# Kernel optimization log

Measured on AMD Instinct MI355X. Metric: run time of the kernel, lower is better.

## Reference

```python
import jax, jax.numpy as jnp
import numpy as np

B, S, D = 4, 2048, 1024
NEG = 1e9


def setup_inputs() -> dict:
    key = jax.random.key(0)
    ks = jax.random.split(key, 4)
    scale = 1.0 / np.sqrt(D)  # glorot-ish init scale for stability
    x = jax.random.normal(ks[0], (B, S, D), dtype=jnp.float32)
    Wq = jax.random.normal(ks[1], (D, D), dtype=jnp.float32) * scale
    Wk = jax.random.normal(ks[2], (D, D), dtype=jnp.float32) * scale
    Wv = jax.random.normal(ks[3], (D, D), dtype=jnp.float32) * scale
    bq = jnp.zeros((D,), jnp.float32)
    bk = jnp.zeros((D,), jnp.float32)
    bv = jnp.zeros((D,), jnp.float32)
    return {"x": x, "Wq": Wq, "bq": bq, "Wk": Wk, "bk": bk, "Wv": Wv, "bv": bv}


def reference(x, Wq, bq, Wk, bk, Wv, bv):
    # Dense projections (single head, no 1/sqrt(d) scaling, matching source)
    q = x @ Wq + bq                      # [B,S,D]
    k = x @ Wk + bk                      # [B,S,D]
    v = x @ Wv + bv                      # [B,S,D]
    scores = jnp.einsum('bqd,bkd->bqk', q, k)   # [B,S,S]
    seq = scores.shape[-1]
    mask = jnp.tril(jnp.ones((seq, seq), scores.dtype))  # lower-triangular causal
    scores = scores * mask - NEG * (1.0 - mask)
    weights = jax.nn.softmax(scores, axis=-1)
    return jnp.einsum('bqk,bkd->bqd', weights, v)
```

## Files before the change

kernel.cpp:

```cpp
#include <hip/hip_runtime.h>

typedef float f32x4  __attribute__((ext_vector_type(4)));
typedef _Float16 f16x8  __attribute__((ext_vector_type(8)));
typedef _Float16 f16x4v __attribute__((ext_vector_type(4)));
typedef _Float16 f16x8v __attribute__((ext_vector_type(8)));

__device__ inline void load_lds16(const _Float16* g, _Float16* l) {
    __builtin_amdgcn_global_load_lds((const __attribute__((address_space(1))) void*)g,
                                     (__attribute__((address_space(3))) void*)l, 16, 0, 0);
}

__global__ __launch_bounds__(256)
void convert_h(const float* __restrict__ X, _Float16* __restrict__ H, long n4)
{
    long i = (long)blockIdx.x * 256 + threadIdx.x;
    if (i >= n4) return;
    f32x4 v = ((const f32x4*)X)[i];
    f16x4v h;
#pragma unroll
    for (int k = 0; k < 4; ++k) h[k] = (_Float16)v[k];
    ((f16x4v*)H)[i] = h;
}

__global__ __launch_bounds__(256)
void transpose_w3(const float* __restrict__ Wq, const float* __restrict__ Wk,
                  const float* __restrict__ Wv,
                  _Float16* __restrict__ W2, _Float16* __restrict__ Wvt, int D)
{
    const int z = blockIdx.z;
    const float* W = (z == 0) ? Wq : (z == 1) ? Wk : Wv;

    __shared__ float t[32][33];
    const int tid = threadIdx.x;
    const int bx = blockIdx.x * 32, by = blockIdx.y * 32;
    const int c = tid & 31, r0 = tid >> 5;
#pragma unroll
    for (int r = r0; r < 32; r += 8)
        t[r][c] = W[(long)(by + r) * D + bx + c];
    __syncthreads();
#pragma unroll
    for (int r = r0; r < 32; r += 8) {
        float v = t[c][r];
        _Float16 h = (_Float16)v;
        if (z < 2) {
            const long nrow = (long)z * D + bx + r;
            W2[nrow * 2 * D + by + c]     = h;
            W2[nrow * 2 * D + D + by + c] = (_Float16)(v - (float)h);
        } else {
            Wvt[(long)(bx + r) * D + by + c] = h;
        }
    }
}

#define STAGES_T(NTHR, NQ, gb, ld, base0, kbase, dst)                           \
    {                                                                           \
        _Pragma("unroll")                                                       \
        for (int q_ = 0; q_ < (NQ); ++q_) {                                     \
            const int p_ = q_ * (NTHR) + tid;                                   \
            const int rp_ = p_ >> 3;                                            \
            const int gl_ = (p_ & 7) ^ (rp_ & 7);                               \
            const int row_ = rp_ + ((gl_ >> 2) << 7);                           \
            load_lds16((gb) + (long)((base0) + row_) * (ld) + (kbase) +         \
                           ((gl_ & 3) << 3),                                    \
                       (dst) + p_ * 8);                                         \
        }                                                                       \
    }

__global__ __launch_bounds__(512)
void proj8(const _Float16* __restrict__ x_h, const _Float16* __restrict__ W2,
           const _Float16* __restrict__ Wvt,
           _Float16* __restrict__ Q_h, _Float16* __restrict__ Khl,
           _Float16* __restrict__ Vt,
           const float* __restrict__ bq, const float* __restrict__ bk,
           const float* __restrict__ bv)
{
    constexpr int D = 1024, SEQ = 2048;
    __shared__ __align__(16) _Float16 lds[65536];

    const int orig = blockIdx.x;
    const bool isV = orig >= 256;
    int ct, rt, ldb, NT2;
    const _Float16* Bb;
    if (!isV) {
        const int x = orig & 7, i = orig >> 3;
        rt = x * 4 + (i & 3);  ct = i >> 2;
        Bb = W2;  ldb = 2 * D; NT2 = 64;
    } else {
        const int o = orig - 256, x = o & 7, i = o >> 3;
        rt = x * 4 + (i & 3);  ct = i >> 2;
        Bb = Wvt; ldb = D;     NT2 = 32;
    }
    const int row0 = rt * 256, col0 = ct * 256;

    const int tid = threadIdx.x;
    const int wave = tid >> 6, lane = tid & 63, l16 = lane & 15, quad = lane >> 4;
    const int wmh = (wave >> 2) * 128;
    const int wn  = (wave & 3) * 64;
    const int ahalf = (wave >> 2) << 2;

    STAGES_T(512, 2, x_h, D, row0, 0,  lds);
    STAGES_T(512, 2, Bb, ldb, col0, 0, lds + 32768);
    STAGES_T(512, 2, x_h, D, row0, 32, lds + 8192);
    STAGES_T(512, 2, Bb, ldb, col0, 32, lds + 32768 + 8192);
    asm volatile("s_waitcnt vmcnt(4)" ::: "memory");
    __builtin_amdgcn_s_barrier();

    f32x4 acc[8][4] = {};

    for (int s = 0; s < NT2; ++s) {
        _Float16* Asl = lds + (s & 3) * 8192;
        _Float16* Bsl = lds + 32768 + (s & 3) * 8192;
        const bool pf = (s + 2 < NT2);
        const int kA2 = ((s + 2) * 32) & (D - 1);
        const int kB2 = (s + 2) * 32;

        f16x8 b[4], a0[4];
#pragma unroll
        for (int j = 0; j < 4; ++j) {
            const int nr = wn + j * 16 + l16;
            const int rpb = nr & 127;
            const int gpb = ((((nr >> 7) << 2) | quad) ^ (rpb & 7));
            b[j] = *(const f16x8*)&Bsl[rpb * 64 + gpb * 8];
        }
#pragma unroll
        for (int il = 0; il < 4; ++il) {
            const int rp = il * 16 + l16;
            const int gpa = ((ahalf | quad) ^ (rp & 7));
            a0[il] = *(const f16x8*)&Asl[rp * 64 + gpa * 8];
        }
        if (pf) STAGES_T(512, 2, x_h, D, row0, kA2, lds + ((s + 2) & 3) * 8192);
        __builtin_amdgcn_s_setprio(1);
#pragma unroll
        for (int il = 0; il < 4; ++il)
#pragma unroll
            for (int j = 0; j < 4; ++j)
                acc[il][j] = __builtin_amdgcn_mfma_f32_16x16x32_f16(
                    a0[il], b[j], acc[il][j], 0, 0, 0);
        __builtin_amdgcn_s_setprio(0);

        f16x8 a1[4];
#pragma unroll
        for (int il = 0; il < 4; ++il) {
            const int rp = (il + 4) * 16 + l16;
            const int gpa = ((ahalf | quad) ^ (rp & 7));
            a1[il] = *(const f16x8*)&Asl[rp * 64 + gpa * 8];
        }
        if (pf) STAGES_T(512, 2, Bb, ldb, col0, kB2, lds + 32768 + ((s + 2) & 3) * 8192);
        __builtin_amdgcn_s_setprio(1);
#pragma unroll
        for (int il = 0; il < 4; ++il)
#pragma unroll
            for (int j = 0; j < 4; ++j)
                acc[4 + il][j] = __builtin_amdgcn_mfma_f32_16x16x32_f16(
                    a1[il], b[j], acc[4 + il][j], 0, 0, 0);
        __builtin_amdgcn_s_setprio(0);

        if (pf)                asm volatile("s_waitcnt vmcnt(4)" ::: "memory");
        else if (s + 2 == NT2) asm volatile("s_waitcnt vmcnt(0)" ::: "memory");
        __builtin_amdgcn_s_barrier();
    }

    if (!isV) {
        const bool isQ = ct < 4;
        const float* bias = isQ ? bq : bk;
#pragma unroll
        for (int j = 0; j < 4; ++j) {
            const int colg = col0 + wn + j * 16 + l16;
            const int cc = isQ ? colg : colg - D;
            const float bval = bias[cc];
#pragma unroll
            for (int i = 0; i < 8; ++i) {
                const int rb = row0 + wmh + i * 16 + quad * 4;
#pragma unroll
                for (int r = 0; r < 4; ++r) {
                    const float v = acc[i][j][r] + bval;
                    const _Float16 h = (_Float16)v;
                    if (isQ) {
                        Q_h[(long)(rb + r) * D + cc] = h;
                    } else {
                        Khl[(long)(rb + r) * 2048 + cc] = h;
                        Khl[(long)(rb + r) * 2048 + 1024 + cc] = (_Float16)(v - (float)h);
                    }
                }
            }
        }
    } else {
        _Float16* sVt = lds;
#pragma unroll
        for (int j = 0; j < 4; ++j) {
            const int cl = wn + j * 16 + l16;
            const float bval = bv[col0 + cl];
#pragma unroll
            for (int i = 0; i < 8; ++i) {
                f16x4v pk;
#pragma unroll
                for (int r = 0; r < 4; ++r) pk[r] = (_Float16)(acc[i][j][r] + bval);
                const int rowb = wmh * 2 + i * 32 + quad * 8;
                const int sb = cl * 512 + (rowb ^ ((cl & 31) << 4));
                *(f16x4v*)((char*)sVt + sb) = pk;
            }
        }
        __syncthreads();
        const int bb = row0 >> 11;
        const int s0 = row0 & (SEQ - 1);
        for (int idx = tid; idx < 8192; idx += 512) {
            const int cl = idx >> 5, r8 = idx & 31;
            const int sb = cl * 512 + ((r8 * 16) ^ ((cl & 31) << 4));
            f16x8v v = *(const f16x8v*)&((char*)sVt)[sb];
            *(f16x8v*)&Vt[((long)bb * D + col0 + cl) * SEQ + s0 + r8 * 8] = v;
        }
    }
}

__global__ __launch_bounds__(512)
void gemm_sc(const _Float16* __restrict__ Q, const _Float16* __restrict__ Khl,
             float* __restrict__ Sc)
{
    constexpr int D = 1024, S = 2048;
    __shared__ __align__(16) _Float16 lds[65536];

    const int bz = blockIdx.y;
    const int t = blockIdx.x;
    int rt = (int)((sqrtf(8.0f * t + 1.0f) - 1.0f) * 0.5f);
    while (rt * (rt + 1) / 2 > t) --rt;
    while ((rt + 1) * (rt + 2) / 2 <= t) ++rt;
    const int ct = t - rt * (rt + 1) / 2;

    const _Float16* gA = Q + (long)bz * S * D;
    const _Float16* gB = Khl + (long)bz * S * 2048;
    const int row0 = rt * 256, col0 = ct * 256;
    constexpr int NT2 = 64;

    const int tid = threadIdx.x;
    const int wave = tid >> 6, lane = tid & 63, l16 = lane & 15, quad = lane >> 4;
    const int wmh = (wave >> 2) * 128;
    const int wn  = (wave & 3) * 64;
    const int ahalf = (wave >> 2) << 2;

    STAGES_T(512, 2, gA, D, row0, 0,  lds);
    STAGES_T(512, 2, gB, 2048, col0, 0, lds + 32768);
    STAGES_T(512, 2, gA, D, row0, 32, lds + 8192);
    STAGES_T(512, 2, gB, 2048, col0, 32, lds + 32768 + 8192);
    asm volatile("s_waitcnt vmcnt(4)" ::: "memory");
    __builtin_amdgcn_s_barrier();

    f32x4 acc[8][4] = {};

    for (int s = 0; s < NT2; ++s) {
        _Float16* Asl = lds + (s & 3) * 8192;
        _Float16* Bsl = lds + 32768 + (s & 3) * 8192;
        const bool pf = (s + 2 < NT2);
        const int kA2 = ((s + 2) * 32) & (D - 1);
        const int kB2 = (s + 2) * 32;

        f16x8 b[4], a0[4];
#pragma unroll
        for (int j = 0; j < 4; ++j) {
            const int nr = wn + j * 16 + l16;
            const int rpb = nr & 127;
            const int gpb = ((((nr >> 7) << 2) | quad) ^ (rpb & 7));
            b[j] = *(const f16x8*)&Bsl[rpb * 64 + gpb * 8];
        }
#pragma unroll
        for (int il = 0; il < 4; ++il) {
            const int rp = il * 16 + l16;
            const int gpa = ((ahalf | quad) ^ (rp & 7));
            a0[il] = *(const f16x8*)&Asl[rp * 64 + gpa * 8];
        }
        if (pf) STAGES_T(512, 2, gA, D, row0, kA2, lds + ((s + 2) & 3) * 8192);
        __builtin_amdgcn_s_setprio(1);
#pragma unroll
        for (int il = 0; il < 4; ++il)
#pragma unroll
            for (int j = 0; j < 4; ++j)
                acc[il][j] = __builtin_amdgcn_mfma_f32_16x16x32_f16(
                    a0[il], b[j], acc[il][j], 0, 0, 0);
        __builtin_amdgcn_s_setprio(0);

        f16x8 a1[4];
#pragma unroll
        for (int il = 0; il < 4; ++il) {
            const int rp = (il + 4) * 16 + l16;
            const int gpa = ((ahalf | quad) ^ (rp & 7));
            a1[il] = *(const f16x8*)&Asl[rp * 64 + gpa * 8];
        }
        if (pf) STAGES_T(512, 2, gB, 2048, col0, kB2, lds + 32768 + ((s + 2) & 3) * 8192);
        __builtin_amdgcn_s_setprio(1);
#pragma unroll
        for (int il = 0; il < 4; ++il)
#pragma unroll
            for (int j = 0; j < 4; ++j)
                acc[4 + il][j] = __builtin_amdgcn_mfma_f32_16x16x32_f16(
                    a1[il], b[j], acc[4 + il][j], 0, 0, 0);
        __builtin_amdgcn_s_setprio(0);

        if (pf)                asm volatile("s_waitcnt vmcnt(4)" ::: "memory");
        else if (s + 2 == NT2) asm volatile("s_waitcnt vmcnt(0)" ::: "memory");
        __builtin_amdgcn_s_barrier();
    }

    float* cf = Sc + (long)bz * S * S;
#pragma unroll
    for (int j = 0; j < 4; ++j) {
        const int col = col0 + wn + j * 16 + l16;
#pragma unroll
        for (int i = 0; i < 8; ++i) {
            const int rb = row0 + wmh + i * 16 + quad * 4;
#pragma unroll
            for (int r = 0; r < 4; ++r)
                cf[(long)(rb + r) * S + col] = acc[i][j][r];
        }
    }
}

__global__ __launch_bounds__(256)
void gemm_pv(const _Float16* __restrict__ P, const _Float16* __restrict__ Vt,
             float* __restrict__ Out)
{
    constexpr int D = 1024, S = 2048;
    __shared__ __align__(16) _Float16 lds[49152];

    const int rt = 7 - (int)blockIdx.x;
    const int ct = blockIdx.y;
    const int bz = blockIdx.z;
    const _Float16* gA = P + (long)bz * S * S;
    const _Float16* gB = Vt + (long)bz * D * S;
    const int row0 = rt * 256, col0 = ct * 128;
    const int NT2 = (rt + 1) * 8;

    const int tid = threadIdx.x;
    const int wave = tid >> 6, lane = tid & 63, l16 = lane & 15, quad = lane >> 4;
    const int wmh = (wave >> 1) * 128;
    const int wn  = (wave & 1) * 64;
    const int ahalf = (wave >> 1) << 2;

#define STAGEB_PV(kbase, dst)                                                   \
    {                                                                           \
        _Pragma("unroll")                                                       \
        for (int q_ = 0; q_ < 2; ++q_) {                                        \
            const int p_ = q_ * 256 + tid;                                      \
            const int rp_ = p_ >> 3;                                            \
            const int gl_ = (p_ & 7) ^ (rp_ & 7);                               \
            const int row_ = rp_ + ((gl_ >> 2) << 6);                           \
            load_lds16(gB + (long)(col0 + row_) * S + (kbase) +                 \
                           ((gl_ & 3) << 3),                                    \
                       (dst) + p_ * 8);                                         \
        }                                                                       \
    }

    STAGES_T(256, 4, gA, S, row0, 0,  lds);
    STAGEB_PV(0, lds + 32768);
    STAGES_T(256, 4, gA, S, row0, 32, lds + 8192);
    STAGEB_PV(32, lds + 32768 + 4096);
    asm volatile("s_waitcnt vmcnt(6)" ::: "memory");
    __builtin_amdgcn_s_barrier();

    f32x4 acc[8][4] = {};

    for (int s = 0; s < NT2; ++s) {
        _Float16* Asl = lds + (s & 3) * 8192;
        _Float16* Bsl = lds + 32768 + (s & 3) * 4096;
        const bool pf = (s + 2 < NT2);
        const int k2 = (s + 2) * 32;

        f16x8 b[4], a[8];
#pragma unroll
        for (int j = 0; j < 4; ++j) {
            const int nr = wn + j * 16 + l16;
            const int rpb = nr & 63;
            const int gpb = ((((nr >> 6) << 2) | quad) ^ (rpb & 7));
            b[j] = *(const f16x8*)&Bsl[rpb * 64 + gpb * 8];
        }
#pragma unroll
        for (int il = 0; il < 8; ++il) {
            const int rp = il * 16 + l16;
            const int gpa = ((ahalf | quad) ^ (rp & 7));
            a[il] = *(const f16x8*)&Asl[rp * 64 + gpa * 8];
        }
        if (pf) {
            STAGES_T(256, 4, gA, S, row0, k2, lds + ((s + 2) & 3) * 8192);
            STAGEB_PV(k2, lds + 32768 + ((s + 2) & 3) * 4096);
        }
        __builtin_amdgcn_s_setprio(1);
#pragma unroll
        for (int il = 0; il < 8; ++il)
#pragma unroll
            for (int j = 0; j < 4; ++j)
                acc[il][j] = __builtin_amdgcn_mfma_f32_16x16x32_f16(
                    a[il], b[j], acc[il][j], 0, 0, 0);
        __builtin_amdgcn_s_setprio(0);

        if (pf)                asm volatile("s_waitcnt vmcnt(6)" ::: "memory");
        else if (s + 2 == NT2) asm volatile("s_waitcnt vmcnt(0)" ::: "memory");
        __builtin_amdgcn_s_barrier();
    }

    float* cf = Out + (long)bz * S * D;
#pragma unroll
    for (int j = 0; j < 4; ++j) {
        const int col = col0 + wn + j * 16 + l16;
#pragma unroll
        for (int i = 0; i < 8; ++i) {
            const int rb = row0 + wmh + i * 16 + quad * 4;
#pragma unroll
            for (int r = 0; r < 4; ++r)
                cf[(long)(rb + r) * D + col] = acc[i][j][r];
        }
    }
#undef STAGEB_PV
}

__global__ __launch_bounds__(256)
void softmax_kernel(const float* __restrict__ Sc, _Float16* __restrict__ P, int seq)
{
    const int r = blockIdx.x, b = blockIdx.y;
    const float* row = Sc + ((long)b * seq + r) * seq;
    _Float16* prow = P + ((long)b * seq + r) * seq;
    const int tid = threadIdx.x;
    const int cmax = ((r >> 8) + 1) << 8;
    const int c0 = tid * 8;

    float v[8];
    f32x4 v0, v1;
    if (c0 <= r) {
        const f32x4* rp = (const f32x4*)row;
        v0 = rp[tid * 2];
        v1 = rp[tid * 2 + 1];
    } else {
        v0 = (f32x4)(-3.0e38f);
        v1 = (f32x4)(-3.0e38f);
    }
    float lmax = -3.0e38f;
#pragma unroll
    for (int k = 0; k < 4; ++k) {
        v[k]     = (c0 + k     <= r) ? v0[k] : -3.0e38f;
        v[k + 4] = (c0 + k + 4 <= r) ? v1[k] : -3.0e38f;
    }
#pragma unroll
    for (int k = 0; k < 8; ++k) lmax = fmaxf(lmax, v[k]);

    __shared__ float red[256];
    red[tid] = lmax; __syncthreads();
    for (int s = 128; s > 0; s >>= 1) {
        if (tid < s) red[tid] = fmaxf(red[tid], red[tid + s]);
        __syncthreads();
    }
    const float m = red[0];
    __syncthreads();

    float lsum = 0.0f;
#pragma unroll
    for (int k = 0; k < 8; ++k) {
        float e = (v[k] > -1.0e38f) ? __expf(v[k] - m) : 0.0f;
        v[k] = e;
        lsum += e;
    }
    red[tid] = lsum; __syncthreads();
    for (int s = 128; s > 0; s >>= 1) {
        if (tid < s) red[tid] += red[tid + s];
        __syncthreads();
    }
    const float inv = 1.0f / red[0];

    if (c0 < cmax) {
        f16x8v o;
#pragma unroll
        for (int k = 0; k < 8; ++k) o[k] = (_Float16)(v[k] * inv);
        ((f16x8v*)prow)[tid] = o;
    }
}

extern "C" void kernel_launch(void* const* d_in, const int* in_sizes, int n_in,
                              void* d_out, int out_size, void* d_ws, size_t ws_size,
                              hipStream_t stream)
{
    constexpr int B = 4, S = 2048, D = 1024;
    constexpr long MB = 1024 * 1024;
    const float* x  = (const float*)d_in[0];
    const float* Wq = (const float*)d_in[1];
    const float* bq = (const float*)d_in[2];
    const float* Wk = (const float*)d_in[3];
    const float* bk = (const float*)d_in[4];
    const float* Wv = (const float*)d_in[5];
    const float* bv = (const float*)d_in[6];
    float* out = (float*)d_out;

    char* ws = (char*)d_ws;
    _Float16* x_h   = (_Float16*)(ws + 0);
    _Float16* W2    = (_Float16*)(ws + 16 * MB);
    _Float16* Wvt_h = (_Float16*)(ws + 24 * MB);
    float*    Sc    = (float*)(ws + 0);
    _Float16* Q_h   = (_Float16*)(ws + 64 * MB);
    _Float16* Khl   = (_Float16*)(ws + 80 * MB);
    _Float16* Vt    = (_Float16*)(ws + 112 * MB);
    _Float16* P     = (_Float16*)(ws + 128 * MB);

    const int M = B * S;
    dim3 blk(256);

    convert_h<<<(M * D / 4 + 255) / 256, blk, 0, stream>>>(x, x_h, (long)M * D / 4);
    transpose_w3<<<dim3(D / 32, D / 32, 3), blk, 0, stream>>>(
        Wq, Wk, Wv, W2, Wvt_h, D);

    proj8<<<dim3(384), dim3(512), 0, stream>>>(
        x_h, W2, Wvt_h, Q_h, Khl, Vt, bq, bk, bv);

    gemm_sc<<<dim3(36, B), dim3(512), 0, stream>>>(Q_h, Khl, Sc);

    softmax_kernel<<<dim3(S, B), blk, 0, stream>>>(Sc, P, S);

    gemm_pv<<<dim3(8, 8, B), dim3(256), 0, stream>>>(P, Vt, out);
}
```

Baseline: 317.6 us.

## Split fused projection into separate QK and V kernels with balanced grids

The single proj8 launch, which mixed 256 long QK tiles (64 k-steps) with 128 short V tiles (32 k-steps) in one grid, becomes two kernels. projQK keeps the 512-thread 256x256 tiling. projV uses 256 threads with 256x128 tiles, giving 256 blocks that reuse the gemm_pv style pipeline and write the transposed V through LDS in two halves. The aim is to remove load imbalance and the tail left by the heterogeneous grid, at the cost of an extra launch and a second pass reading x_h.

```diff
diff --git a/kernel.cpp b/kernel.cpp
--- a/kernel.cpp
+++ b/kernel.cpp
@@ -53,7 +53,7 @@
 }
 
 #define STAGES_T(NTHR, NQ, gb, ld, base0, kbase, dst)                           \
-    {                                                                           \
+    do {                                                                        \
         _Pragma("unroll")                                                       \
         for (int q_ = 0; q_ < (NQ); ++q_) {                                     \
             const int p_ = q_ * (NTHR) + tid;                                   \
@@ -64,33 +64,35 @@
                            ((gl_ & 3) << 3),                                    \
                        (dst) + p_ * 8);                                         \
         }                                                                       \
-    }
+    } while (0)
+
+#define STAGEB128(gb, ld, base0, kbase, dst)                                    \
+    do {                                                                        \
+        _Pragma("unroll")                                                       \
+        for (int q_ = 0; q_ < 2; ++q_) {                                        \
+            const int p_ = q_ * 256 + tid;                                      \
+            const int rp_ = p_ >> 3;                                            \
+            const int gl_ = (p_ & 7) ^ (rp_ & 7);                               \
+            const int row_ = rp_ + ((gl_ >> 2) << 6);                           \
+            load_lds16((gb) + (long)((base0) + row_) * (ld) + (kbase) +         \
+                           ((gl_ & 3) << 3),                                    \
+                       (dst) + p_ * 8);                                         \
+        }                                                                       \
+    } while (0)
 
 __global__ __launch_bounds__(512)
-void proj8(const _Float16* __restrict__ x_h, const _Float16* __restrict__ W2,
-           const _Float16* __restrict__ Wvt,
-           _Float16* __restrict__ Q_h, _Float16* __restrict__ Khl,
-           _Float16* __restrict__ Vt,
-           const float* __restrict__ bq, const float* __restrict__ bk,
-           const float* __restrict__ bv)
-{
-    constexpr int D = 1024, SEQ = 2048;
+void projQK(const _Float16* __restrict__ x_h, const _Float16* __restrict__ W2,
+            _Float16* __restrict__ Q_h, _Float16* __restrict__ Khl,
+            const float* __restrict__ bq, const float* __restrict__ bk)
+{
+    constexpr int D = 1024;
     __shared__ __align__(16) _Float16 lds[65536];
 
     const int orig = blockIdx.x;
-    const bool isV = orig >= 256;
-    int ct, rt, ldb, NT2;
-    const _Float16* Bb;
-    if (!isV) {
-        const int x = orig & 7, i = orig >> 3;
-        rt = x * 4 + (i & 3);  ct = i >> 2;
-        Bb = W2;  ldb = 2 * D; NT2 = 64;
-    } else {
-        const int o = orig - 256, x = o & 7, i = o >> 3;
-        rt = x * 4 + (i & 3);  ct = i >> 2;
-        Bb = Wvt; ldb = D;     NT2 = 32;
-    }
+    const int x = orig & 7, i = orig >> 3;
+    const int rt = x * 4 + (i & 3), ct = i >> 2;
     const int row0 = rt * 256, col0 = ct * 256;
+    constexpr int NT2 = 64;
 
     const int tid = threadIdx.x;
     const int wave = tid >> 6, lane = tid & 63, l16 = lane & 15, quad = lane >> 4;
@@ -99,9 +101,9 @@
     const int ahalf = (wave >> 2) << 2;
 
     STAGES_T(512, 2, x_h, D, row0, 0,  lds);
-    STAGES_T(512, 2, Bb, ldb, col0, 0, lds + 32768);
+    STAGES_T(512, 2, W2, 2048, col0, 0, lds + 32768);
     STAGES_T(512, 2, x_h, D, row0, 32, lds + 8192);
-    STAGES_T(512, 2, Bb, ldb, col0, 32, lds + 32768 + 8192);
+    STAGES_T(512, 2, W2, 2048, col0, 32, lds + 32768 + 8192);
     asm volatile("s_waitcnt vmcnt(4)" ::: "memory");
     __builtin_amdgcn_s_barrier();
 
@@ -145,7 +147,7 @@
             const int gpa = ((ahalf | quad) ^ (rp & 7));
             a1[il] = *(const f16x8*)&Asl[rp * 64 + gpa * 8];
         }
-        if (pf) STAGES_T(512, 2, Bb, ldb, col0, kB2, lds + 32768 + ((s + 2) & 3) * 8192);
+        if (pf) STAGES_T(512, 2, W2, 2048, col0, kB2, lds + 32768 + ((s + 2) & 3) * 8192);
         __builtin_amdgcn_s_setprio(1);
 #pragma unroll
         for (int il = 0; il < 4; ++il)
@@ -160,55 +162,128 @@
         __builtin_amdgcn_s_barrier();
     }
 
-    if (!isV) {
-        const bool isQ = ct < 4;
-        const float* bias = isQ ? bq : bk;
-#pragma unroll
-        for (int j = 0; j < 4; ++j) {
-            const int colg = col0 + wn + j * 16 + l16;
-            const int cc = isQ ? colg : colg - D;
-            const float bval = bias[cc];
-#pragma unroll
-            for (int i = 0; i < 8; ++i) {
-                const int rb = row0 + wmh + i * 16 + quad * 4;
-#pragma unroll
-                for (int r = 0; r < 4; ++r) {
-                    const float v = acc[i][j][r] + bval;
-                    const _Float16 h = (_Float16)v;
-                    if (isQ) {
-                        Q_h[(long)(rb + r) * D + cc] = h;
-                    } else {
-                        Khl[(long)(rb + r) * 2048 + cc] = h;
-                        Khl[(long)(rb + r) * 2048 + 1024 + cc] = (_Float16)(v - (float)h);
-                    }
+    const bool isQ = ct < 4;
+    const float* bias = isQ ? bq : bk;
+#pragma unroll
+    for (int j = 0; j < 4; ++j) {
+        const int colg = col0 + wn + j * 16 + l16;
+        const int cc = isQ ? colg : colg - D;
+        const float bval = bias[cc];
+#pragma unroll
+        for (int i = 0; i < 8; ++i) {
+            const int rb = row0 + wmh + i * 16 + quad * 4;
+#pragma unroll
+            for (int r = 0; r < 4; ++r) {
+                const float v = acc[i][j][r] + bval;
+                const _Float16 h = (_Float16)v;
+                if (isQ) {
+                    Q_h[(long)(rb + r) * D + cc] = h;
+                } else {
+                    Khl[(long)(rb + r) * 2048 + cc] = h;
+                    Khl[(long)(rb + r) * 2048 + 1024 + cc] = (_Float16)(v - (float)h);
                 }
             }
         }
-    } else {
-        _Float16* sVt = lds;
+    }
+}
+
+__global__ __launch_bounds__(256)
+void projV(const _Float16* __restrict__ x_h, const _Float16* __restrict__ Wvt,
+           _Float16* __restrict__ Vt, const float* __restrict__ bv)
+{
+    constexpr int D = 1024, S = 2048;
+    __shared__ __align__(16) _Float16 lds[49152];
+
+    const int o = blockIdx.x;
+    const int rtg = o & 31, ctv = o >> 5;
+    const int row0 = rtg * 256, col0 = ctv * 128;
+    constexpr int NT2 = 32;
+
+    const int tid = threadIdx.x;
+    const int wave = tid >> 6, lane = tid & 63, l16 = lane & 15, quad = lane >> 4;
+    const int wmh = (wave >> 1) * 128;
+    const int wn  = (wave & 1) * 64;
+    const int ahalf = (wave >> 1) << 2;
+
+    STAGES_T(256, 4, x_h, D, row0, 0,  lds);
+    STAGEB128(Wvt, D, col0, 0, lds + 32768);
+    STAGES_T(256, 4, x_h, D, row0, 32, lds + 8192);
+    STAGEB128(Wvt, D, col0, 32, lds + 32768 + 4096);
+    asm volatile("s_waitcnt vmcnt(6)" ::: "memory");
+    __builtin_amdgcn_s_barrier();
+
+    f32x4 acc[8][4] = {};
+
+    for (int s = 0; s < NT2; ++s) {
+        _Float16* Asl = lds + (s & 3) * 8192;
+        _Float16* Bsl = lds + 32768 + (s & 3) * 4096;
+        const bool pf = (s + 2 < NT2);
+        const int k2 = (s + 2) * 32;
+
+        f16x8 b[4], a[8];
 #pragma unroll
         for (int j = 0; j < 4; ++j) {
-            const int cl = wn + j * 16 + l16;
-            const float bval = bv[col0 + cl];
-#pragma unroll
-            for (int i = 0; i < 8; ++i) {
-                f16x4v pk;
-#pragma unroll
-                for (int r = 0; r < 4; ++r) pk[r] = (_Float16)(acc[i][j][r] + bval);
-                const int rowb = wmh * 2 + i * 32 + quad * 8;
-                const int sb = cl * 512 + (rowb ^ ((cl & 31) << 4));
-                *(f16x4v*)((char*)sVt + sb) = pk;
+            const int nr = wn + j * 16 + l16;
+            const int rpb = nr & 63;
+            const int gpb = ((((nr >> 6) << 2) | quad) ^ (rpb & 7));
+            b[j] = *(const f16x8*)&Bsl[rpb * 64 + gpb * 8];
+        }
+#pragma unroll
+        for (int il = 0; il < 8; ++il) {
+            const int rp = il * 16 + l16;
+            const int gpa = ((ahalf | quad) ^ (rp & 7));
+            a[il] = *(const f16x8*)&Asl[rp * 64 + gpa * 8];
+        }
+        if (pf) {
+            STAGES_T(256, 4, x_h, D, row0, k2, lds + ((s + 2) & 3) * 8192);
+            STAGEB128(Wvt, D, col0, k2, lds + 32768 + ((s + 2) & 3) * 4096);
+        }
+        __builtin_amdgcn_s_setprio(1);
+#pragma unroll
+        for (int il = 0; il < 8; ++il)
+#pragma unroll
+            for (int j = 0; j < 4; ++j)
+                acc[il][j] = __builtin_amdgcn_mfma_f32_16x16x32_f16(
+                    a[il], b[j], acc[il][j], 0, 0, 0);
+        __builtin_amdgcn_s_setprio(0);
+
+        if (pf)                asm volatile("s_waitcnt vmcnt(6)" ::: "memory");
+        else if (s + 2 == NT2) asm volatile("s_waitcnt vmcnt(0)" ::: "memory");
+        __builtin_amdgcn_s_barrier();
+    }
+
+    _Float16* sVt = lds;
+    const int bb = row0 >> 11;
+    const int s0 = row0 & (S - 1);
+    __syncthreads();
+#pragma unroll
+    for (int ch = 0; ch < 2; ++ch) {
+        if ((wave & 1) == ch) {
+#pragma unroll
+            for (int j = 0; j < 4; ++j) {
+                const int cl2 = j * 16 + l16;
+                const float bval = bv[col0 + ch * 64 + cl2];
+#pragma unroll
+                for (int i = 0; i < 8; ++i) {
+                    f16x4v pk;
+#pragma unroll
+                    for (int r = 0; r < 4; ++r)
+                        pk[r] = (_Float16)(acc[i][j][r] + bval);
+                    const int rowb = wmh * 2 + i * 32 + quad * 8;
+                    const int sb = cl2 * 512 + (rowb ^ ((cl2 & 31) << 4));
+                    *(f16x4v*)((char*)sVt + sb) = pk;
+                }
             }
         }
         __syncthreads();
-        const int bb = row0 >> 11;
-        const int s0 = row0 & (SEQ - 1);
-        for (int idx = tid; idx < 8192; idx += 512) {
-            const int cl = idx >> 5, r8 = idx & 31;
-            const int sb = cl * 512 + ((r8 * 16) ^ ((cl & 31) << 4));
-            f16x8v v = *(const f16x8v*)&((char*)sVt)[sb];
-            *(f16x8v*)&Vt[((long)bb * D + col0 + cl) * SEQ + s0 + r8 * 8] = v;
-        }
+        for (int idx = tid; idx < 2048; idx += 256) {
+            const int cl2 = idx >> 5, r8 = idx & 31;
+            const int sb = cl2 * 512 + ((r8 * 16) ^ ((cl2 & 31) << 4));
+            f16x8v v = *(const f16x8v*)((char*)sVt + sb);
+            *(f16x8v*)&Vt[((long)bb * D + col0 + ch * 64 + cl2) * S +
+                          s0 + r8 * 8] = v;
+        }
+        __syncthreads();
     }
 }
 
@@ -334,24 +409,10 @@
     const int wn  = (wave & 1) * 64;
     const int ahalf = (wave >> 1) << 2;
 
-#define STAGEB_PV(kbase, dst)                                                   \
-    {                                                                           \
-        _Pragma("unroll")                                                       \
-        for (int q_ = 0; q_ < 2; ++q_) {                                        \
-            const int p_ = q_ * 256 + tid;                                      \
-            const int rp_ = p_ >> 3;                                            \
-            const int gl_ = (p_ & 7) ^ (rp_ & 7);                               \
-            const int row_ = rp_ + ((gl_ >> 2) << 6);                           \
-            load_lds16(gB + (long)(col0 + row_) * S + (kbase) +                 \
-                           ((gl_ & 3) << 3),                                    \
-                       (dst) + p_ * 8);                                         \
-        }                                                                       \
-    }
-
     STAGES_T(256, 4, gA, S, row0, 0,  lds);
-    STAGEB_PV(0, lds + 32768);
+    STAGEB128(gB, S, col0, 0, lds + 32768);
     STAGES_T(256, 4, gA, S, row0, 32, lds + 8192);
-    STAGEB_PV(32, lds + 32768 + 4096);
+    STAGEB128(gB, S, col0, 32, lds + 32768 + 4096);
     asm volatile("s_waitcnt vmcnt(6)" ::: "memory");
     __builtin_amdgcn_s_barrier();
 
@@ -379,7 +440,7 @@
         }
         if (pf) {
             STAGES_T(256, 4, gA, S, row0, k2, lds + ((s + 2) & 3) * 8192);
-            STAGEB_PV(k2, lds + 32768 + ((s + 2) & 3) * 4096);
+            STAGEB128(gB, S, col0, k2, lds + 32768 + ((s + 2) & 3) * 4096);
         }
         __builtin_amdgcn_s_setprio(1);
 #pragma unroll
@@ -407,7 +468,6 @@
                 cf[(long)(rb + r) * D + col] = acc[i][j][r];
         }
     }
-#undef STAGEB_PV
 }
 
 __global__ __launch_bounds__(256)
@@ -486,28 +546,23 @@
     float* out = (float*)d_out;
 
     char* ws = (char*)d_ws;
-    _Float16* x_h   = (_Float16*)(ws + 0);
-    _Float16* W2    = (_Float16*)(ws + 16 * MB);
-    _Float16* Wvt_h = (_Float16*)(ws + 24 * MB);
-    float*    Sc    = (float*)(ws + 0);
-    _Float16* Q_h   = (_Float16*)(ws + 64 * MB);
-    _Float16* Khl   = (_Float16*)(ws + 80 * MB);
-    _Float16* Vt    = (_Float16*)(ws + 112 * MB);
-    _Float16* P     = (_Float16*)(ws + 128 * MB);
+    _Float16* x_h = (_Float16*)(ws + 0);
+    _Float16* W2  = (_Float16*)(ws + 16 * MB);
+    _Float16* Wvt = (_Float16*)(ws + 24 * MB);
+    float*    Sc  = (float*)(ws + 0);
+    _Float16* Q_h = (_Float16*)(ws + 64 * MB);
+    _Float16* Khl = (_Float16*)(ws + 80 * MB);
+    _Float16* Vt  = (_Float16*)(ws + 112 * MB);
+    _Float16* P   = (_Float16*)(ws + 128 * MB);
 
     const int M = B * S;
     dim3 blk(256);
 
     convert_h<<<(M * D / 4 + 255) / 256, blk, 0, stream>>>(x, x_h, (long)M * D / 4);
-    transpose_w3<<<dim3(D / 32, D / 32, 3), blk, 0, stream>>>(
-        Wq, Wk, Wv, W2, Wvt_h, D);
-
-    proj8<<<dim3(384), dim3(512), 0, stream>>>(
-        x_h, W2, Wvt_h, Q_h, Khl, Vt, bq, bk, bv);
-
+    transpose_w3<<<dim3(D / 32, D / 32, 3), blk, 0, stream>>>(Wq, Wk, Wv, W2, Wvt, D);
+    projQK<<<dim3(256), dim3(512), 0, stream>>>(x_h, W2, Q_h, Khl, bq, bk);
+    projV<<<dim3(256), blk, 0, stream>>>(x_h, Wvt, Vt, bv);
     gemm_sc<<<dim3(36, B), dim3(512), 0, stream>>>(Q_h, Khl, Sc);
-
     softmax_kernel<<<dim3(S, B), blk, 0, stream>>>(Sc, P, S);
-
-    gemm_pv<<<dim3(8, 8, B), dim3(256), 0, stream>>>(P, Vt, out);
-}
+    gemm_pv<<<dim3(8, 8, B), blk, 0, stream>>>(P, Vt, out);
+}
```

After: 311.9 us. Within noise of the previous version (-1.8%).
